# Optimization experiments

Hardware: AMD Instinct MI355X
Metric: run time of the kernel (lower is better)

## Reference

```python
import jax, jax.numpy as jnp
import numpy as np

HID = 400
K = 10  # attention mixture components


def _lstm_cell(x, h, c, Wih, Whh, b):
    # torch gate order: i, f, g, o
    g = x @ Wih.T + h @ Whh.T + b
    i, f, gg, o = jnp.split(g, 4, axis=-1)
    c = jax.nn.sigmoid(f) * c + jax.nn.sigmoid(i) * jnp.tanh(gg)
    h = jax.nn.sigmoid(o) * jnp.tanh(c)
    return h, c


def setup_inputs() -> dict:
    key = jax.random.key(0)
    ks = jax.random.split(key, 14)
    B, T, U, D = 64, 600, 64, 60
    s = 0.08  # keep exp() in attention numerically tame
    strokes = jax.random.normal(ks[0], (B, T, 3), dtype=jnp.float32)
    ids = jax.random.randint(ks[1], (B, U), 0, D)
    onehots = jax.nn.one_hot(ids, D, dtype=jnp.float32)
    text_mask = jnp.ones((B, U), dtype=jnp.float32)
    W_ih1 = jax.random.normal(ks[2], (4 * HID, D + 3)) * s
    W_hh1 = jax.random.normal(ks[3], (4 * HID, HID)) * s
    b1 = jax.random.normal(ks[4], (4 * HID,)) * s  # b_ih + b_hh combined
    W_win = jax.random.normal(ks[5], (3 * K, HID)) * s
    b_win = jax.random.normal(ks[6], (3 * K,)) * s
    W_ih2 = jax.random.normal(ks[7], (4 * HID, 3 + D + HID)) * s
    W_hh2 = jax.random.normal(ks[8], (4 * HID, HID)) * s
    b2 = jax.random.normal(ks[9], (4 * HID,)) * s
    W_fc = jax.random.normal(ks[10], (121, 2 * HID)) * s
    b_fc = jax.random.normal(ks[11], (121,)) * s
    return {"strokes": strokes, "onehots": onehots, "text_mask": text_mask,
            "W_ih1": W_ih1, "W_hh1": W_hh1, "b1": b1,
            "W_win": W_win, "b_win": b_win,
            "W_ih2": W_ih2, "W_hh2": W_hh2, "b2": b2,
            "W_fc": W_fc, "b_fc": b_fc}


def reference(strokes, onehots, text_mask, W_ih1, W_hh1, b1, W_win, b_win,
              W_ih2, W_hh2, b2, W_fc, b_fc):
    B, T, _ = strokes.shape
    U = onehots.shape[1]
    u = jnp.arange(U, dtype=jnp.float32)

    def step1(carry, x_t):
        h0, c0, kappa, w = carry
        h0, c0 = _lstm_cell(jnp.concatenate([x_t, w], -1), h0, c0, W_ih1, W_hh1, b1)
        p = jnp.exp(h0 @ W_win.T + b_win)              # [B, 3K]
        alpha, beta, kap = jnp.split(p, 3, axis=-1)    # each [B, K]
        kappa = kappa + kap
        diff = kappa[:, None, :] - u[None, :, None]    # [B, U, K]
        phi = jnp.sum(alpha[:, None, :] * jnp.exp(-beta[:, None, :] * diff * diff), -1)
        phi = phi * text_mask                          # [B, U]
        w = jnp.einsum('bu,bud->bd', phi, onehots)     # [B, D]
        return (h0, c0, kappa, w), (h0, w, phi)

    z = jnp.zeros((B, HID), jnp.float32)
    init = (z, z, jnp.zeros((B, K), jnp.float32), onehots[:, 0, :])
    (h0f, c0f, kappa_f, w_f), (H1, Wt, Phi) = jax.lax.scan(step1, init, strokes.transpose(1, 0, 2))
    lstm1_out = H1.transpose(1, 0, 2)                  # [B, T, 400]
    attn_out = Wt.transpose(1, 0, 2)                   # [B, T, D]
    phi_last = Phi[-1]

    x2 = jnp.concatenate([strokes, attn_out, lstm1_out], -1)  # [B, T, 463]

    def step2(carry, x_t):
        h, c = carry
        h, c = _lstm_cell(x_t, h, c, W_ih2, W_hh2, b2)
        return (h, c), h

    (h1f, c1f), H2 = jax.lax.scan(step2, (z, z), x2.transpose(1, 0, 2))
    lstm2_out = H2.transpose(1, 0, 2)                  # [B, T, 400]

    out = jnp.concatenate([lstm1_out, lstm2_out], -1) @ W_fc.T + b_fc  # [B, T, 121]
    mu, log_sigma, pi, rho, eos = jnp.split(out, [40, 80, 100, 120], axis=-1)
    rho = jnp.tanh(rho)
    pi = jax.nn.softmax(pi, axis=-1)
    eos = jax.nn.sigmoid(-eos)
    mu = mu.reshape(B, T, 20, 2)
    sigma = log_sigma.reshape(B, T, 20, 2)  # original returns raw log-sigma reshaped
    return (pi, mu, sigma, rho, eos, w_f, kappa_f, phi_last, h0f, c0f, h1f, c1f)
```

## Files before the change

kernel.cpp:

```cpp
#include <hip/hip_runtime.h>
#include <hip/hip_bf16.h>
#include <math.h>

#define HIDN 400
#define KK   10
#define UU   64
#define DD   60
#define TT   600
#define FCIN 800
#define FCOUT 121

#define NH1  100
#define NH2  100
#define NWBK 32
#define WBAT 2
#define TOTB 232
#define THR  1024
#define NWAVE 16
#define CB   16
#define PSTR 68

#define SLOT1 25600
#define SLOTW 3840

#define PI_OFF    0
#define MU_OFF    768000
#define SIG_OFF   2304000
#define RHO_OFF   3840000
#define EOS_OFF   4608000
#define WF_OFF    4646400
#define KAPPA_OFF 4650240
#define PHI_OFF   4650880
#define H0F_OFF   4654976
#define C0F_OFF   4680576
#define H1F_OFF   4706176
#define C1F_OFF   4731776

#define WS_H1T   0
#define WS_H2T   15385600
#define WS_WHT   30771200
#define WS_XST   33079040
#define WS_WALL1 33194240
#define WS_WALL2 33935040
#define WS_WFCT  35315840
#define WS_CNT   35412640

#define CAI(i,g) ((((i)&7)*13+(g))*16)
#define CWI(i,g) (1664 + (((i)&7)*4+(g))*16)
#define CHI(i,g) (2176 + (((i)&7)*13+(g))*16)
#define CNT_INTS 3840

#define SMEM_F 32512

__device__ __forceinline__ float sigm(float x){ return 1.0f/(1.0f + expf(-x)); }
__device__ __forceinline__ int tgtn(int i, int n){ return n*((i>>3)+1); }

__device__ __forceinline__ void st_agent(float* p, float v){
  __hip_atomic_store(p, v, __ATOMIC_RELAXED, __HIP_MEMORY_SCOPE_AGENT);
}
__device__ __forceinline__ int ld_agent_i(const int* p){
  return __hip_atomic_load(p, __ATOMIC_RELAXED, __HIP_MEMORY_SCOPE_AGENT);
}
__device__ __forceinline__ void arrive(int* p){
  __hip_atomic_fetch_add(p, 1, __ATOMIC_RELAXED, __HIP_MEMORY_SCOPE_AGENT);
}
__device__ __forceinline__ void spin_ge(const int* w, int tgt){
  if (ld_agent_i(w) >= tgt) return;
  do { __builtin_amdgcn_s_sleep(1); } while (ld_agent_i(w) < tgt);
}

__global__ void prep_init(const float* __restrict__ onehots, const float* __restrict__ strokes,
                          float* __restrict__ H1t, float* __restrict__ H2t,
                          float* __restrict__ Wh,  float* __restrict__ XST,
                          int* __restrict__ cnts){
  int idx = blockIdx.x*blockDim.x + threadIdx.x;
  if (idx < SLOT1){ H1t[idx] = 0.f; H2t[idx] = 0.f; }
  if (idx < SLOTW){
    int d = idx >> 6, b = idx & 63;
    Wh[idx] = onehots[b*(UU*DD) + d];
  }
  if (idx < TT*3*64){
    int t = idx/192, rem = idx%192, comp = rem/64, b = rem%64;
    XST[idx] = strokes[(b*TT + t)*3 + comp];
  }
  if (idx < CNT_INTS) cnts[idx] = 0;
}

__global__ void prep_wall(const float* __restrict__ Wih1, const float* __restrict__ Whh1,
                          const float* __restrict__ Wih2, const float* __restrict__ Whh2,
                          float* __restrict__ WALL1, float* __restrict__ WALL2){
  int idx = blockIdx.x*blockDim.x + threadIdx.x;
  if (idx < 640000){
    int g = idx/400, k = idx%400;
    int q = g/400, j = g%400, pp = j>>2, c = 4*q + (j&3);
    WALL1[((size_t)pp*463 + k)*CB + c] = Whh1[idx];
  } else if (idx < 740800){
    int s = idx - 640000;
    int g = s/63, col = s%63;
    int q = g/400, j = g%400, pp = j>>2, c = 4*q + (j&3);
    int r = (col < 3) ? (460 + col) : (400 + col - 3);
    WALL1[((size_t)pp*463 + r)*CB + c] = Wih1[s];
  } else if (idx < 1380800){
    int s = idx - 740800;
    int g = s/400, k = s%400;
    int q = g/400, j = g%400, pp = j>>2, c = 4*q + (j&3);
    WALL2[((size_t)pp*863 + 400 + k)*CB + c] = Whh2[s];
  } else if (idx < 2121600){
    int s = idx - 1380800;
    int g = s/463, col = s%463;
    int q = g/400, j = g%400, pp = j>>2, c = 4*q + (j&3);
    int r = (col<3) ? (860+col) : (col<63 ? (800+col-3) : (col-63));
    WALL2[((size_t)pp*863 + r)*CB + c] = Wih2[s];
  }
}

__global__ void prep_wfc(const float* __restrict__ Wfc, float* __restrict__ WfcT){
  int idx = blockIdx.x*blockDim.x + threadIdx.x;
  if (idx >= FCIN*FCOUT) return;
  int k = idx / FCOUT, j = idx - k*FCOUT;
  WfcT[idx] = Wfc[j*FCIN + k];
}

__device__ __forceinline__ void gemv16(const float* __restrict__ x,
                                       const float* __restrict__ w,
                                       int n, int bg4, int cg4, float acc[16]){
  #pragma unroll 4
  for (int k=0;k<n;++k){
    const float4 xv = *(const float4*)(x + k*64 + bg4);
    const float4 wv = *(const float4*)(w + k*CB + cg4);
    acc[0]  = fmaf(wv.x, xv.x, acc[0]);
    acc[1]  = fmaf(wv.x, xv.y, acc[1]);
    acc[2]  = fmaf(wv.x, xv.z, acc[2]);
    acc[3]  = fmaf(wv.x, xv.w, acc[3]);
    acc[4]  = fmaf(wv.y, xv.x, acc[4]);
    acc[5]  = fmaf(wv.y, xv.y, acc[5]);
    acc[6]  = fmaf(wv.y, xv.z, acc[6]);
    acc[7]  = fmaf(wv.y, xv.w, acc[7]);
    acc[8]  = fmaf(wv.z, xv.x, acc[8]);
    acc[9]  = fmaf(wv.z, xv.y, acc[9]);
    acc[10] = fmaf(wv.z, xv.z, acc[10]);
    acc[11] = fmaf(wv.z, xv.w, acc[11]);
    acc[12] = fmaf(wv.w, xv.x, acc[12]);
    acc[13] = fmaf(wv.w, xv.y, acc[13]);
    acc[14] = fmaf(wv.w, xv.z, acc[14]);
    acc[15] = fmaf(wv.w, xv.w, acc[15]);
  }
}

__global__ __launch_bounds__(THR) void recurrent_kernel(
    const float* __restrict__ Wwin, const float* __restrict__ bwin,
    const float* __restrict__ b1g,  const float* __restrict__ b2g,
    const float* __restrict__ tmask,const float* __restrict__ onehots,
    const float* __restrict__ WALL1,const float* __restrict__ WALL2,
    float* __restrict__ H1t,        float* __restrict__ H2t,
    float* __restrict__ Wh,         const float* __restrict__ XST,
    int* __restrict__ cnts,         float* __restrict__ outp)
{
  const int p   = blockIdx.x;
  const int tid = threadIdx.x;
  __shared__ float SM[SMEM_F];

  if (p < NH1){
    const int wave = tid >> 6, lane = tid & 63;
    const int bg4  = (lane & 15) * 4;
    const int cg4  = (lane >> 4) * 4;
    float* WL1 = SM;          float* PART = SM + 7408;
    float* GRED= SM + 24816;  float* CS   = SM + 25840;
    float* BS  = SM + 26096;

    for (int idx = tid; idx < 463*CB; idx += THR) WL1[idx] = WALL1[(size_t)p*463*CB + idx];
    if (tid < 16){ int q = tid>>2, u = tid&3; BS[tid] = b1g[q*HIDN + 4*p + u]; }
    if (tid < 256) CS[tid] = 0.f;
    __syncthreads();

    for (int i = 0; i < TT; ++i){
      if (i >= 1){
        if (tid < 13) spin_ge(&cnts[CAI(i-1, tid)], tgtn(i-1, tid==12?4:8));
        asm volatile("" ::: "memory");
        __syncthreads();
      }
      float acc[16];
      #pragma unroll
      for (int z=0; z<16; ++z) acc[z] = 0.f;
      {
        const float* __restrict__ H1prev = H1t + (size_t)i*SLOT1;
        int k0 = wave*26, k1 = min(k0 + 26, 403);
        { int ka = k0, kb = min(k1, 400);
          if (kb > ka) gemv16(H1prev + ka*64, WL1 + ka*CB, kb-ka, bg4, cg4, acc); }
        { int ka = max(k0,400), kb = k1;
          if (kb > ka) gemv16(XST + i*192 + (ka-400)*64, WL1 + (460+(ka-400))*CB, kb-ka, bg4, cg4, acc); }
      }
      if (i >= 1){
        if (tid < 4) spin_ge(&cnts[CWI(i-1, tid)], tgtn(i-1, 8));
        asm volatile("" ::: "memory");
        __syncthreads();
      }
      {
        const float* __restrict__ Whp = Wh + (size_t)i*SLOTW;
        int k0 = wave*4, k1 = min(k0 + 4, 60);
        if (k1 > k0) gemv16(Whp + k0*64, WL1 + (400+k0)*CB, k1-k0, bg4, cg4, acc);
      }
      #pragma unroll
      for (int cc=0; cc<4; ++cc)
        *(float4*)&PART[(wave*16 + cg4 + cc)*PSTR + bg4] =
          make_float4(acc[cc*4+0], acc[cc*4+1], acc[cc*4+2], acc[cc*4+3]);
      __syncthreads();
      {
        int c = tid>>6, b = tid&63; float s = 0.f;
        #pragma unroll
        for (int w16=0; w16<NWAVE; ++w16) s += PART[(w16*16 + c)*PSTR + b];
        GRED[c*64 + b] = s;
      }
      __syncthreads();
      if (tid < 256){
        int u = tid>>6, b = tid&63, j = 4*p + u;
        float gi = GRED[( 0+u)*64+b] + BS[ 0+u];
        float gf = GRED[( 4+u)*64+b] + BS[ 4+u];
        float gg = GRED[( 8+u)*64+b] + BS[ 8+u];
        float go = GRED[(12+u)*64+b] + BS[12+u];
        float c_ = sigm(gf)*CS[u*64+b] + sigm(gi)*tanhf(gg);
        float h_ = sigm(go)*tanhf(c_);
        CS[u*64+b] = c_;
        st_agent(&H1t[(size_t)(i+1)*SLOT1 + j*64 + b], h_);
        if (i == TT-1){ outp[H0F_OFF + b*HIDN + j] = h_; outp[C0F_OFF + b*HIDN + j] = c_; }
      }
      __syncthreads();
      if (tid == 0) arrive(&cnts[CAI(i, p>>3)]);
    }
  } else if (p < NH1 + NH2){
    const int q2 = p - NH1;
    const int wave = tid >> 6, lane = tid & 63;
    const int bg4  = (lane & 15) * 4;
    const int cg4  = (lane >> 4) * 4;
    float* WL2 = SM;          float* PART = SM + 13808;
    float* GRED= SM + 31216;  float* CS   = SM + 32240;
    float* BS  = SM + 32496;

    for (int idx = tid; idx < 863*CB; idx += THR) WL2[idx] = WALL2[(size_t)q2*863*CB + idx];
    if (tid < 16){ int q = tid>>2, u = tid&3; BS[tid] = b2g[q*HIDN + 4*q2 + u]; }
    if (tid < 256) CS[tid] = 0.f;
    __syncthreads();

    for (int t2 = 0; t2 < TT; ++t2){
      if (tid < 13) spin_ge(&cnts[CAI(t2, tid)], tgtn(t2, tid==12?4:8));
      else if (tid >= 64 && tid < 68) spin_ge(&cnts[CWI(t2, tid-64)], tgtn(t2, 8));
      asm volatile("" ::: "memory");
      __syncthreads();
      float acc[16];
      #pragma unroll
      for (int z=0; z<16; ++z) acc[z] = 0.f;
      {
        const float* __restrict__ H1v = H1t + (size_t)(t2+1)*SLOT1;
        const float* __restrict__ Whv = Wh  + (size_t)(t2+1)*SLOTW;
        int k0 = wave*29, k1 = min(k0 + 29, 463);
        { int ka = k0, kb = min(k1, 400);
          if (kb > ka) gemv16(H1v + ka*64, WL2 + ka*CB, kb-ka, bg4, cg4, acc); }
        { int ka = max(k0,400), kb = min(k1, 460);
          if (kb > ka) gemv16(Whv + (ka-400)*64, WL2 + (800+(ka-400))*CB, kb-ka, bg4, cg4, acc); }
        { int ka = max(k0,460), kb = k1;
          if (kb > ka) gemv16(XST + t2*192 + (ka-460)*64, WL2 + (860+(ka-460))*CB, kb-ka, bg4, cg4, acc); }
      }
      if (t2 >= 1){
        if (tid < 13) spin_ge(&cnts[CHI(t2-1, tid)], tgtn(t2-1, tid==12?4:8));
        asm volatile("" ::: "memory");
        __syncthreads();
      }
      {
        const float* __restrict__ H2v = H2t + (size_t)t2*SLOT1;
        int k0 = wave*25, k1 = min(k0 + 25, 400);
        if (k1 > k0) gemv16(H2v + k0*64, WL2 + (400+k0)*CB, k1-k0, bg4, cg4, acc);
      }
      #pragma unroll
      for (int cc=0; cc<4; ++cc)
        *(float4*)&PART[(wave*16 + cg4 + cc)*PSTR + bg4] =
          make_float4(acc[cc*4+0], acc[cc*4+1], acc[cc*4+2], acc[cc*4+3]);
      __syncthreads();
      {
        int c = tid>>6, b = tid&63; float s = 0.f;
        #pragma unroll
        for (int w16=0; w16<NWAVE; ++w16) s += PART[(w16*16 + c)*PSTR + b];
        GRED[c*64 + b] = s;
      }
      __syncthreads();
      if (tid < 256){
        int u = tid>>6, b = tid&63, j = 4*q2 + u;
        float gi = GRED[( 0+u)*64+b] + BS[ 0+u];
        float gf = GRED[( 4+u)*64+b] + BS[ 4+u];
        float gg = GRED[( 8+u)*64+b] + BS[ 8+u];
        float go = GRED[(12+u)*64+b] + BS[12+u];
        float c_ = sigm(gf)*CS[u*64+b] + sigm(gi)*tanhf(gg);
        float h_ = sigm(go)*tanhf(c_);
        CS[u*64+b] = c_;
        st_agent(&H2t[(size_t)(t2+1)*SLOT1 + j*64 + b], h_);
        if (t2 == TT-1){ outp[H1F_OFF + b*HIDN + j] = h_; outp[C1F_OFF + b*HIDN + j] = c_; }
      }
      __syncthreads();
      if (tid == 0) arrive(&cnts[CHI(t2, q2>>3)]);
    }
  } else {
    const int wb = p - NH1 - NH2;
    const int b0 = wb * WBAT;
    float* WWT = SM;          float* ONE = SM + 13200;
    float* H1S = SM + 20880;  float* TMS = SM + 22080;
    float* PW  = SM + 22208;  float* KAP = SM + 22272;
    float* PHI = SM + 22304;

    for (int idx = tid; idx < 30*400; idx += THR){
      int j = idx/400, k = idx - j*400;
      WWT[k*33 + j] = Wwin[idx];
    }
    for (int idx = tid; idx < WBAT*UU*DD; idx += THR) ONE[idx] = onehots[b0*(UU*DD) + idx];
    if (tid < WBAT*UU) TMS[tid] = tmask[b0*UU + tid];
    if (tid < WBAT*16) KAP[tid] = 0.f;
    __syncthreads();

    for (int i = 0; i < TT; ++i){
      if (tid < 13) spin_ge(&cnts[CAI(i, tid)], tgtn(i, tid==12?4:8));
      asm volatile("" ::: "memory");
      __syncthreads();
      const float* __restrict__ H1now = H1t + (size_t)(i+1)*SLOT1;
      if (tid < 800){
        int bb = tid / 400, k = tid - bb*400;
        H1S[k*3 + bb] = H1now[k*64 + b0 + bb];
      }
      __syncthreads();
      if (tid < 960){
        int ks = tid & 15, pair = tid >> 4;
        int b = pair / 30, j = pair - b*30;
        float s = 0.f;
        #pragma unroll
        for (int kk = 0; kk < 25; ++kk){
          int k = ks*25 + kk;
          s = fmaf(H1S[k*3 + b], WWT[k*33 + j], s);
        }
        s += __shfl_down(s, 8, 16);
        s += __shfl_down(s, 4, 16);
        s += __shfl_down(s, 2, 16);
        s += __shfl_down(s, 1, 16);
        if (ks == 0) PW[b*32 + j] = expf(s + bwin[j]);
      }
      __syncthreads();
      if (tid < WBAT*KK){
        int b = tid/KK, k = tid - b*KK;
        KAP[b*16 + k] += PW[b*32 + 20 + k];
      }
      __syncthreads();
      if (tid < WBAT*UU){
        int b = tid >> 6, u = tid & 63;
        float uf = (float)u, s = 0.f;
        #pragma unroll
        for (int q = 0; q < KK; ++q){
          float d = KAP[b*16 + q] - uf;
          s = fmaf(PW[b*32 + q], expf(-PW[b*32 + 10 + q]*d*d), s);
        }
        s *= TMS[b*64 + u];
        PHI[b*64 + u] = s;
        if (i == TT-1) outp[PHI_OFF + (b0+b)*UU + u] = s;
      }
      __syncthreads();
      if (tid < WBAT*DD){
        int b = tid/DD, d = tid - b*DD;
        float s = 0.f;
        #pragma unroll 8
        for (int u = 0; u < UU; ++u) s = fmaf(PHI[b*64 + u], ONE[b*(UU*DD) + u*DD + d], s);
        st_agent(&Wh[(size_t)(i+1)*SLOTW + d*64 + b0 + b], s);
        if (i == TT-1) outp[WF_OFF + (b0+b)*DD + d] = s;
      }
      if (i == TT-1 && tid < WBAT*KK){
        int b = tid/KK, k = tid - b*KK;
        outp[KAPPA_OFF + (b0+b)*KK + k] = KAP[b*16 + k];
      }
      __syncthreads();
      if (tid == 0) arrive(&cnts[CWI(i, wb>>3)]);
    }
  }
}

__global__ __launch_bounds__(128) void fc2_kernel(
    const float* __restrict__ H1t, const float* __restrict__ H2t,
    const float* __restrict__ WfcT, const float* __restrict__ bfc,
    float* __restrict__ outp)
{
  const int t   = blockIdx.x;
  const int tid = threadIdx.x;
  __shared__ float Xs[8][64];
  __shared__ float OUT[FCOUT][65];
  float acc[64];
  #pragma unroll
  for (int b=0;b<64;++b) acc[b]=0.f;
  const float* __restrict__ base1 = H1t + (size_t)(t+1)*SLOT1;
  const float* __restrict__ base2 = H2t + (size_t)(t+1)*SLOT1;

  for (int kb=0; kb<100; ++kb){
    __syncthreads();
    #pragma unroll
    for (int e=0;e<4;++e){
      int idx = e*128 + tid;
      int row = idx>>6, b = idx&63;
      int k = kb*8 + row;
      Xs[row][b] = (k<400) ? base1[k*64+b] : base2[(k-400)*64+b];
    }
    __syncthreads();
    if (tid < FCOUT){
      #pragma unroll
      for (int kk=0;kk<8;++kk){
        float wv = WfcT[(kb*8+kk)*FCOUT + tid];
        #pragma unroll
        for (int b4=0;b4<16;++b4){
          float4 xv = *(const float4*)&Xs[kk][b4*4];
          acc[b4*4+0] = fmaf(wv, xv.x, acc[b4*4+0]);
          acc[b4*4+1] = fmaf(wv, xv.y, acc[b4*4+1]);
          acc[b4*4+2] = fmaf(wv, xv.z, acc[b4*4+2]);
          acc[b4*4+3] = fmaf(wv, xv.w, acc[b4*4+3]);
        }
      }
    }
  }
  if (tid < FCOUT){
    float bj = bfc[tid];
    #pragma unroll
    for (int b=0;b<64;++b) OUT[tid][b] = acc[b] + bj;
  }
  __syncthreads();
  if (tid < 64){
    const int b = tid;
    const size_t pos = (size_t)b*TT + t;
    for (int j=0;j<40;++j) outp[MU_OFF  + pos*40 + j] = OUT[j][b];
    for (int j=0;j<40;++j) outp[SIG_OFF + pos*40 + j] = OUT[40+j][b];
    float m = -1e30f;
    for (int q=0;q<20;++q) m = fmaxf(m, OUT[80+q][b]);
    float e[20], s=0.f;
    for (int q=0;q<20;++q){ e[q]=expf(OUT[80+q][b]-m); s+=e[q]; }
    float inv = 1.f/s;
    for (int q=0;q<20;++q) outp[PI_OFF  + pos*20 + q] = e[q]*inv;
    for (int q=0;q<20;++q) outp[RHO_OFF + pos*20 + q] = tanhf(OUT[100+q][b]);
    outp[EOS_OFF + pos] = 1.0f/(1.0f + expf(OUT[120][b]));
  }
}

extern "C" void kernel_launch(void* const* d_in, const int* in_sizes, int n_in,
                              void* d_out, int out_size, void* d_ws, size_t ws_size,
                              hipStream_t stream){
  (void)in_sizes; (void)n_in; (void)out_size; (void)ws_size;
  const float* strokes = (const float*)d_in[0];
  const float* onehots = (const float*)d_in[1];
  const float* tmask   = (const float*)d_in[2];
  const float* Wih1    = (const float*)d_in[3];
  const float* Whh1    = (const float*)d_in[4];
  const float* b1      = (const float*)d_in[5];
  const float* Wwin    = (const float*)d_in[6];
  const float* bwin    = (const float*)d_in[7];
  const float* Wih2    = (const float*)d_in[8];
  const float* Whh2    = (const float*)d_in[9];
  const float* b2      = (const float*)d_in[10];
  const float* Wfc     = (const float*)d_in[11];
  const float* bfc     = (const float*)d_in[12];

  float* ws    = (float*)d_ws;
  float* outp  = (float*)d_out;
  float* H1t   = ws + WS_H1T;
  float* H2t   = ws + WS_H2T;
  float* Wh    = ws + WS_WHT;
  float* XST   = ws + WS_XST;
  float* WALL1 = ws + WS_WALL1;
  float* WALL2 = ws + WS_WALL2;
  float* WfcT  = ws + WS_WFCT;
  int*   cnts  = (int*)(ws + WS_CNT);

  hipLaunchKernelGGL(prep_init, dim3((TT*3*64 + 255)/256), dim3(256), 0, stream,
                     onehots, strokes, H1t, H2t, Wh, XST, cnts);
  hipLaunchKernelGGL(prep_wall, dim3((2121600 + 255)/256), dim3(256), 0, stream,
                     Wih1, Whh1, Wih2, Whh2, WALL1, WALL2);
  hipLaunchKernelGGL(prep_wfc, dim3((FCIN*FCOUT + 255)/256), dim3(256), 0, stream,
                     Wfc, WfcT);

  hipLaunchKernelGGL(recurrent_kernel, dim3(TOTB), dim3(THR), 0, stream,
                     Wwin, bwin, b1, b2, tmask, onehots, WALL1, WALL2,
                     H1t, H2t, Wh, XST, cnts, outp);

  hipLaunchKernelGGL(fc2_kernel, dim3(TT), dim3(128), 0, stream,
                     H1t, H2t, WfcT, bfc, outp);
}
```

Before: 7.327 ms.

## Use per-wave fine-grained spin waits and batch four sequences per attention block

Replaces the block-wide spin-then-__syncthreads waits with per-wave spins on only the counter groups each wave's k-slice depends on. Each wave can then start its partial GEMV as soon as its own input rows are ready, instead of waiting for the whole hidden vector. The attention-window blocks now handle four batch rows each (16 blocks instead of 32), with a padded one-hot layout, bias cached in shared memory and coalesced output stores. The trade-off is more redundant global polling per wave and more serial work per attention block.

```diff
diff --git a/kernel.cpp b/kernel.cpp
--- a/kernel.cpp
+++ b/kernel.cpp
@@ -12,9 +12,9 @@
 
 #define NH1  100
 #define NH2  100
-#define NWBK 32
-#define WBAT 2
-#define TOTB 232
+#define NWBK 16
+#define WBAT 4
+#define TOTB 216
 #define THR  1024
 #define NWAVE 16
 #define CB   16
@@ -46,14 +46,15 @@
 #define WS_CNT   35412640
 
 #define CAI(i,g) ((((i)&7)*13+(g))*16)
-#define CWI(i,g) (1664 + (((i)&7)*4+(g))*16)
-#define CHI(i,g) (2176 + (((i)&7)*13+(g))*16)
-#define CNT_INTS 3840
+#define CWI(i,g) (1664 + (((i)&7)*2+(g))*16)
+#define CHI(i,g) (1920 + (((i)&7)*13+(g))*16)
+#define CNT_INTS 3584
+#define TGT8(i)  ((((i)>>3)+1)*8)
+#define TGT4(i)  ((((i)>>3)+1)*4)
 
 #define SMEM_F 32512
 
 __device__ __forceinline__ float sigm(float x){ return 1.0f/(1.0f + expf(-x)); }
-__device__ __forceinline__ int tgtn(int i, int n){ return n*((i>>3)+1); }
 
 __device__ __forceinline__ void st_agent(float* p, float v){
   __hip_atomic_store(p, v, __ATOMIC_RELAXED, __HIP_MEMORY_SCOPE_AGENT);
@@ -174,31 +175,35 @@
     __syncthreads();
 
     for (int i = 0; i < TT; ++i){
-      if (i >= 1){
-        if (tid < 13) spin_ge(&cnts[CAI(i-1, tid)], tgtn(i-1, tid==12?4:8));
-        asm volatile("" ::: "memory");
-        __syncthreads();
-      }
       float acc[16];
       #pragma unroll
       for (int z=0; z<16; ++z) acc[z] = 0.f;
+      const int k0 = wave*26, k1 = min(k0 + 26, 403);
+      if (i >= 1){
+        int kh = min(k1, 400);
+        if (kh > k0){
+          int g0 = k0 >> 5, g1 = (kh-1) >> 5;
+          for (int g = g0; g <= g1; ++g)
+            spin_ge(&cnts[CAI(i-1,g)], (g==12) ? TGT4(i-1) : TGT8(i-1));
+          asm volatile("" ::: "memory");
+        }
+      }
       {
         const float* __restrict__ H1prev = H1t + (size_t)i*SLOT1;
-        int k0 = wave*26, k1 = min(k0 + 26, 403);
         { int ka = k0, kb = min(k1, 400);
           if (kb > ka) gemv16(H1prev + ka*64, WL1 + ka*CB, kb-ka, bg4, cg4, acc); }
         { int ka = max(k0,400), kb = k1;
           if (kb > ka) gemv16(XST + i*192 + (ka-400)*64, WL1 + (460+(ka-400))*CB, kb-ka, bg4, cg4, acc); }
       }
       if (i >= 1){
-        if (tid < 4) spin_ge(&cnts[CWI(i-1, tid)], tgtn(i-1, 8));
+        spin_ge(&cnts[CWI(i-1,0)], TGT8(i-1));
+        spin_ge(&cnts[CWI(i-1,1)], TGT8(i-1));
         asm volatile("" ::: "memory");
-        __syncthreads();
       }
       {
         const float* __restrict__ Whp = Wh + (size_t)i*SLOTW;
-        int k0 = wave*4, k1 = min(k0 + 4, 60);
-        if (k1 > k0) gemv16(Whp + k0*64, WL1 + (400+k0)*CB, k1-k0, bg4, cg4, acc);
+        int m0 = wave*4, m1 = min(m0 + 4, 60);
+        if (m1 > m0) gemv16(Whp + m0*64, WL1 + (400+m0)*CB, m1-m0, bg4, cg4, acc);
       }
       #pragma unroll
       for (int cc=0; cc<4; ++cc)
@@ -242,13 +247,12 @@
     __syncthreads();
 
     for (int t2 = 0; t2 < TT; ++t2){
-      if (tid < 13) spin_ge(&cnts[CAI(t2, tid)], tgtn(t2, tid==12?4:8));
-      else if (tid >= 64 && tid < 68) spin_ge(&cnts[CWI(t2, tid-64)], tgtn(t2, 8));
-      asm volatile("" ::: "memory");
-      __syncthreads();
       float acc[16];
       #pragma unroll
       for (int z=0; z<16; ++z) acc[z] = 0.f;
+      spin_ge(&cnts[CWI(t2,0)], TGT8(t2));
+      spin_ge(&cnts[CWI(t2,1)], TGT8(t2));
+      asm volatile("" ::: "memory");
       {
         const float* __restrict__ H1v = H1t + (size_t)(t2+1)*SLOT1;
         const float* __restrict__ Whv = Wh  + (size_t)(t2+1)*SLOTW;
@@ -260,15 +264,16 @@
         { int ka = max(k0,460), kb = k1;
           if (kb > ka) gemv16(XST + t2*192 + (ka-460)*64, WL2 + (860+(ka-460))*CB, kb-ka, bg4, cg4, acc); }
       }
-      if (t2 >= 1){
-        if (tid < 13) spin_ge(&cnts[CHI(t2-1, tid)], tgtn(t2-1, tid==12?4:8));
+      const int m0 = wave*25, m1 = min(m0 + 25, 400);
+      if (t2 >= 1 && m1 > m0){
+        int g0 = m0 >> 5, g1 = (m1-1) >> 5;
+        for (int g = g0; g <= g1; ++g)
+          spin_ge(&cnts[CHI(t2-1,g)], (g==12) ? TGT4(t2-1) : TGT8(t2-1));
         asm volatile("" ::: "memory");
-        __syncthreads();
       }
       {
         const float* __restrict__ H2v = H2t + (size_t)t2*SLOT1;
-        int k0 = wave*25, k1 = min(k0 + 25, 400);
-        if (k1 > k0) gemv16(H2v + k0*64, WL2 + (400+k0)*CB, k1-k0, bg4, cg4, acc);
+        if (m1 > m0) gemv16(H2v + m0*64, WL2 + (400+m0)*CB, m1-m0, bg4, cg4, acc);
       }
       #pragma unroll
       for (int cc=0; cc<4; ++cc)
@@ -300,44 +305,51 @@
   } else {
     const int wb = p - NH1 - NH2;
     const int b0 = wb * WBAT;
+    const int wave = tid >> 6, lane = tid & 63;
     float* WWT = SM;          float* ONE = SM + 13200;
-    float* H1S = SM + 20880;  float* TMS = SM + 22080;
-    float* PW  = SM + 22208;  float* KAP = SM + 22272;
-    float* PHI = SM + 22304;
+    float* H1S = SM + 28848;  float* TMS = SM + 30848;
+    float* PW  = SM + 31104;  float* KAP = SM + 31232;
+    float* PHI = SM + 31296;  float* BWS = SM + 31552;
 
     for (int idx = tid; idx < 30*400; idx += THR){
       int j = idx/400, k = idx - j*400;
       WWT[k*33 + j] = Wwin[idx];
     }
-    for (int idx = tid; idx < WBAT*UU*DD; idx += THR) ONE[idx] = onehots[b0*(UU*DD) + idx];
+    for (int idx = tid; idx < WBAT*UU*DD; idx += THR){
+      int b = idx/3840, rem = idx - b*3840, u = rem/60, d = rem - u*60;
+      ONE[b*3912 + u*61 + d] = onehots[(size_t)(b0+b)*3840 + rem];
+    }
     if (tid < WBAT*UU) TMS[tid] = tmask[b0*UU + tid];
     if (tid < WBAT*16) KAP[tid] = 0.f;
+    if (tid < 30) BWS[tid] = bwin[tid];
     __syncthreads();
 
     for (int i = 0; i < TT; ++i){
-      if (tid < 13) spin_ge(&cnts[CAI(i, tid)], tgtn(i, tid==12?4:8));
-      asm volatile("" ::: "memory");
-      __syncthreads();
       const float* __restrict__ H1now = H1t + (size_t)(i+1)*SLOT1;
-      if (tid < 800){
-        int bb = tid / 400, k = tid - bb*400;
-        H1S[k*3 + bb] = H1now[k*64 + b0 + bb];
+      if (wave < 13){
+        spin_ge(&cnts[CAI(i,wave)], (wave==12) ? TGT4(i) : TGT8(i));
+        asm volatile("" ::: "memory");
+        const int nrows = (wave==12) ? 16 : 32;
+        const int base  = wave*32;
+        for (int idx = lane; idx < nrows*WBAT; idx += 64){
+          int k = base + (idx >> 2), bb = idx & 3;
+          H1S[k*5 + bb] = H1now[k*64 + b0 + bb];
+        }
       }
       __syncthreads();
       if (tid < 960){
-        int ks = tid & 15, pair = tid >> 4;
+        int ks = tid & 7, pair = tid >> 3;
         int b = pair / 30, j = pair - b*30;
         float s = 0.f;
         #pragma unroll
-        for (int kk = 0; kk < 25; ++kk){
-          int k = ks*25 + kk;
-          s = fmaf(H1S[k*3 + b], WWT[k*33 + j], s);
+        for (int kk = 0; kk < 50; ++kk){
+          int k = ks*50 + kk;
+          s = fmaf(H1S[k*5 + b], WWT[k*33 + j], s);
         }
-        s += __shfl_down(s, 8, 16);
-        s += __shfl_down(s, 4, 16);
-        s += __shfl_down(s, 2, 16);
-        s += __shfl_down(s, 1, 16);
-        if (ks == 0) PW[b*32 + j] = expf(s + bwin[j]);
+        s += __shfl_down(s, 4, 8);
+        s += __shfl_down(s, 2, 8);
+        s += __shfl_down(s, 1, 8);
+        if (ks == 0) PW[b*32 + j] = expf(s + BWS[j]);
       }
       __syncthreads();
       if (tid < WBAT*KK){
@@ -359,10 +371,10 @@
       }
       __syncthreads();
       if (tid < WBAT*DD){
-        int b = tid/DD, d = tid - b*DD;
+        int d = tid >> 2, b = tid & 3;
         float s = 0.f;
         #pragma unroll 8
-        for (int u = 0; u < UU; ++u) s = fmaf(PHI[b*64 + u], ONE[b*(UU*DD) + u*DD + d], s);
+        for (int u = 0; u < UU; ++u) s = fmaf(PHI[b*64 + u], ONE[b*3912 + u*61 + d], s);
         st_agent(&Wh[(size_t)(i+1)*SLOTW + d*64 + b0 + b], s);
         if (i == TT-1) outp[WF_OFF + (b0+b)*DD + d] = s;
       }
```

Result: slower. 7.727 ms (+5.5%).

## Overlap dependency waits with GEMV work and use per-wave arrival counters

Applied to the files above, without the earlier changes.

Arrivals on the step counters now happen per wave right after each wave drains its stores, instead of once per block after a block barrier, and the wait targets are scaled to match. In both LSTM blocks one wave is set aside to spin on the window or previous-hidden-state counters while the other 15 waves compute the input GEMV chunk, which removes one block barrier per step. The attention blocks now wait per wave on each group counter and copy only that group's rows as soon as it is ready. The window bias is also cached in shared memory. The changes reduce serialized barrier and spin latency on the critical recurrent path, at the cost of more atomics and a heavier load on the computing waves.

```diff
diff --git a/kernel.cpp b/kernel.cpp
--- a/kernel.cpp
+++ b/kernel.cpp
@@ -49,11 +49,11 @@
 #define CWI(i,g) (1664 + (((i)&7)*4+(g))*16)
 #define CHI(i,g) (2176 + (((i)&7)*13+(g))*16)
 #define CNT_INTS 3840
-
-#define SMEM_F 32512
+#define TGTA8(i) ((((i)>>3)+1)*32)
+#define TGTA4(i) ((((i)>>3)+1)*16)
+#define TGTW(i)  ((((i)>>3)+1)*16)
 
 __device__ __forceinline__ float sigm(float x){ return 1.0f/(1.0f + expf(-x)); }
-__device__ __forceinline__ int tgtn(int i, int n){ return n*((i>>3)+1); }
 
 __device__ __forceinline__ void st_agent(float* p, float v){
   __hip_atomic_store(p, v, __ATOMIC_RELAXED, __HIP_MEMORY_SCOPE_AGENT);
@@ -67,6 +67,10 @@
 __device__ __forceinline__ void spin_ge(const int* w, int tgt){
   if (ld_agent_i(w) >= tgt) return;
   do { __builtin_amdgcn_s_sleep(1); } while (ld_agent_i(w) < tgt);
+}
+__device__ __forceinline__ void wave_drain_arrive(int* cnt, int lane){
+  asm volatile("s_waitcnt vmcnt(0)" ::: "memory");
+  if (lane == 0) arrive(cnt);
 }
 
 __global__ void prep_init(const float* __restrict__ onehots, const float* __restrict__ strokes,
@@ -158,7 +162,7 @@
 {
   const int p   = blockIdx.x;
   const int tid = threadIdx.x;
-  __shared__ float SM[SMEM_F];
+  __shared__ float SM[32512];
 
   if (p < NH1){
     const int wave = tid >> 6, lane = tid & 63;
@@ -175,30 +179,31 @@
 
     for (int i = 0; i < TT; ++i){
       if (i >= 1){
-        if (tid < 13) spin_ge(&cnts[CAI(i-1, tid)], tgtn(i-1, tid==12?4:8));
+        if (tid < 13) spin_ge(&cnts[CAI(i-1, tid)], (tid==12) ? TGTA4(i-1) : TGTA8(i-1));
         asm volatile("" ::: "memory");
         __syncthreads();
       }
       float acc[16];
       #pragma unroll
       for (int z=0; z<16; ++z) acc[z] = 0.f;
-      {
+
+      if (wave < 15){
         const float* __restrict__ H1prev = H1t + (size_t)i*SLOT1;
-        int k0 = wave*26, k1 = min(k0 + 26, 403);
+        int k0 = wave*27, k1 = min(k0 + 27, 403);
         { int ka = k0, kb = min(k1, 400);
           if (kb > ka) gemv16(H1prev + ka*64, WL1 + ka*CB, kb-ka, bg4, cg4, acc); }
         { int ka = max(k0,400), kb = k1;
           if (kb > ka) gemv16(XST + i*192 + (ka-400)*64, WL1 + (460+(ka-400))*CB, kb-ka, bg4, cg4, acc); }
-      }
-      if (i >= 1){
-        if (tid < 4) spin_ge(&cnts[CWI(i-1, tid)], tgtn(i-1, 8));
-        asm volatile("" ::: "memory");
-        __syncthreads();
-      }
+      } else if (i >= 1 && lane < 4){
+        spin_ge(&cnts[CWI(i-1, lane)], TGTW(i-1));
+      }
+      asm volatile("" ::: "memory");
+      __syncthreads();
+
       {
         const float* __restrict__ Whp = Wh + (size_t)i*SLOTW;
-        int k0 = wave*4, k1 = min(k0 + 4, 60);
-        if (k1 > k0) gemv16(Whp + k0*64, WL1 + (400+k0)*CB, k1-k0, bg4, cg4, acc);
+        int m0 = wave*4, m1 = min(m0 + 4, 60);
+        if (m1 > m0) gemv16(Whp + m0*64, WL1 + (400+m0)*CB, m1-m0, bg4, cg4, acc);
       }
       #pragma unroll
       for (int cc=0; cc<4; ++cc)
@@ -223,9 +228,9 @@
         CS[u*64+b] = c_;
         st_agent(&H1t[(size_t)(i+1)*SLOT1 + j*64 + b], h_);
         if (i == TT-1){ outp[H0F_OFF + b*HIDN + j] = h_; outp[C0F_OFF + b*HIDN + j] = c_; }
-      }
-      __syncthreads();
-      if (tid == 0) arrive(&cnts[CAI(i, p>>3)]);
+        wave_drain_arrive(&cnts[CAI(i, p>>3)], lane);
+      }
+      __syncthreads();
     }
   } else if (p < NH1 + NH2){
     const int q2 = p - NH1;
@@ -242,33 +247,34 @@
     __syncthreads();
 
     for (int t2 = 0; t2 < TT; ++t2){
-      if (tid < 13) spin_ge(&cnts[CAI(t2, tid)], tgtn(t2, tid==12?4:8));
-      else if (tid >= 64 && tid < 68) spin_ge(&cnts[CWI(t2, tid-64)], tgtn(t2, 8));
+      if (tid < 13) spin_ge(&cnts[CAI(t2, tid)], (tid==12) ? TGTA4(t2) : TGTA8(t2));
+      else if (tid >= 64 && tid < 68) spin_ge(&cnts[CWI(t2, tid-64)], TGTW(t2));
       asm volatile("" ::: "memory");
       __syncthreads();
       float acc[16];
       #pragma unroll
       for (int z=0; z<16; ++z) acc[z] = 0.f;
-      {
+
+      if (wave < 15){
         const float* __restrict__ H1v = H1t + (size_t)(t2+1)*SLOT1;
         const float* __restrict__ Whv = Wh  + (size_t)(t2+1)*SLOTW;
-        int k0 = wave*29, k1 = min(k0 + 29, 463);
+        int k0 = wave*31, k1 = min(k0 + 31, 463);
         { int ka = k0, kb = min(k1, 400);
           if (kb > ka) gemv16(H1v + ka*64, WL2 + ka*CB, kb-ka, bg4, cg4, acc); }
         { int ka = max(k0,400), kb = min(k1, 460);
           if (kb > ka) gemv16(Whv + (ka-400)*64, WL2 + (800+(ka-400))*CB, kb-ka, bg4, cg4, acc); }
         { int ka = max(k0,460), kb = k1;
           if (kb > ka) gemv16(XST + t2*192 + (ka-460)*64, WL2 + (860+(ka-460))*CB, kb-ka, bg4, cg4, acc); }
-      }
-      if (t2 >= 1){
-        if (tid < 13) spin_ge(&cnts[CHI(t2-1, tid)], tgtn(t2-1, tid==12?4:8));
-        asm volatile("" ::: "memory");
-        __syncthreads();
-      }
+      } else if (t2 >= 1 && lane < 13){
+        spin_ge(&cnts[CHI(t2-1, lane)], (lane==12) ? TGTA4(t2-1) : TGTA8(t2-1));
+      }
+      asm volatile("" ::: "memory");
+      __syncthreads();
+
       {
         const float* __restrict__ H2v = H2t + (size_t)t2*SLOT1;
-        int k0 = wave*25, k1 = min(k0 + 25, 400);
-        if (k1 > k0) gemv16(H2v + k0*64, WL2 + (400+k0)*CB, k1-k0, bg4, cg4, acc);
+        int m0 = wave*25, m1 = min(m0 + 25, 400);
+        if (m1 > m0) gemv16(H2v + m0*64, WL2 + (400+m0)*CB, m1-m0, bg4, cg4, acc);
       }
       #pragma unroll
       for (int cc=0; cc<4; ++cc)
@@ -293,17 +299,18 @@
         CS[u*64+b] = c_;
         st_agent(&H2t[(size_t)(t2+1)*SLOT1 + j*64 + b], h_);
         if (t2 == TT-1){ outp[H1F_OFF + b*HIDN + j] = h_; outp[C1F_OFF + b*HIDN + j] = c_; }
-      }
-      __syncthreads();
-      if (tid == 0) arrive(&cnts[CHI(t2, q2>>3)]);
+        wave_drain_arrive(&cnts[CHI(t2, q2>>3)], lane);
+      }
+      __syncthreads();
     }
   } else {
     const int wb = p - NH1 - NH2;
     const int b0 = wb * WBAT;
+    const int wave = tid >> 6, lane = tid & 63;
     float* WWT = SM;          float* ONE = SM + 13200;
     float* H1S = SM + 20880;  float* TMS = SM + 22080;
     float* PW  = SM + 22208;  float* KAP = SM + 22272;
-    float* PHI = SM + 22304;
+    float* PHI = SM + 22304;  float* BWS = SM + 22432;
 
     for (int idx = tid; idx < 30*400; idx += THR){
       int j = idx/400, k = idx - j*400;
@@ -312,16 +319,21 @@
     for (int idx = tid; idx < WBAT*UU*DD; idx += THR) ONE[idx] = onehots[b0*(UU*DD) + idx];
     if (tid < WBAT*UU) TMS[tid] = tmask[b0*UU + tid];
     if (tid < WBAT*16) KAP[tid] = 0.f;
+    if (tid < 30) BWS[tid] = bwin[tid];
     __syncthreads();
 
     for (int i = 0; i < TT; ++i){
-      if (tid < 13) spin_ge(&cnts[CAI(i, tid)], tgtn(i, tid==12?4:8));
-      asm volatile("" ::: "memory");
-      __syncthreads();
       const float* __restrict__ H1now = H1t + (size_t)(i+1)*SLOT1;
-      if (tid < 800){
-        int bb = tid / 400, k = tid - bb*400;
-        H1S[k*3 + bb] = H1now[k*64 + b0 + bb];
+      if (wave < 13){
+        if (lane == 0) spin_ge(&cnts[CAI(i,wave)], (wave==12) ? TGTA4(i) : TGTA8(i));
+        asm volatile("" ::: "memory");
+        __builtin_amdgcn_wave_barrier();
+        const int nrows = (wave==12) ? 16 : 32;
+        const int base  = wave*32;
+        for (int idx = lane; idx < nrows*WBAT; idx += 64){
+          int k = base + (idx >> 1), bb = idx & 1;
+          H1S[k*3 + bb] = H1now[k*64 + b0 + bb];
+        }
       }
       __syncthreads();
       if (tid < 960){
@@ -337,7 +349,7 @@
         s += __shfl_down(s, 4, 16);
         s += __shfl_down(s, 2, 16);
         s += __shfl_down(s, 1, 16);
-        if (ks == 0) PW[b*32 + j] = expf(s + bwin[j]);
+        if (ks == 0) PW[b*32 + j] = expf(s + BWS[j]);
       }
       __syncthreads();
       if (tid < WBAT*KK){
@@ -365,13 +377,13 @@
         for (int u = 0; u < UU; ++u) s = fmaf(PHI[b*64 + u], ONE[b*(UU*DD) + u*DD + d], s);
         st_agent(&Wh[(size_t)(i+1)*SLOTW + d*64 + b0 + b], s);
         if (i == TT-1) outp[WF_OFF + (b0+b)*DD + d] = s;
+        wave_drain_arrive(&cnts[CWI(i, wb>>3)], lane);
       }
       if (i == TT-1 && tid < WBAT*KK){
         int b = tid/KK, k = tid - b*KK;
         outp[KAPPA_OFF + (b0+b)*KK + k] = KAP[b*16 + k];
       }
       __syncthreads();
-      if (tid == 0) arrive(&cnts[CWI(i, wb>>3)]);
     }
   }
 }
```

Result: slower. 9.074 ms (+23.8%).
